# Optimization experiments

Hardware: AMD Instinct MI355X
Metric: run time of the kernel (lower is better)

Reference implementation:

```python
import jax, jax.numpy as jnp
import numpy as np

BETA = 0.5
THR = 1.0
BN_EPS = 1e-5

@jax.custom_vjp
def spike(x):
    # heaviside fire: spk = 1[x > 0]
    return (x > 0).astype(x.dtype)

def _spike_fwd(x):
    return spike(x), x

def _spike_bwd(x, g):
    # snnTorch surrogate.atan(), alpha=2: grad = (alpha/2) / (1 + (pi/2*alpha*x)^2) = 1/(1+(pi*x)^2)
    return (g / (1.0 + (jnp.pi * x) ** 2),)

spike.defvjp(_spike_fwd, _spike_bwd)

def setup_inputs() -> dict:
    key = jax.random.key(0)
    ks = jax.random.split(key, 6)
    B, T, D, O = 512, 128, 512, 10
    data = jax.random.normal(ks[0], (B, T, D), dtype=jnp.float32)
    # deterministic Dropout(0.5) mask in {0, 2} (scaled by 1/keep_prob), time-major
    u = jax.random.uniform(ks[1], (T, B, D), dtype=jnp.float32)
    drop_mask = (u > 0.5).astype(jnp.float32) * 2.0
    W1 = jax.random.normal(ks[2], (D, D), dtype=jnp.float32) / np.sqrt(D)
    b1 = jax.random.normal(ks[3], (D,), dtype=jnp.float32) * 0.01
    gamma = jnp.ones((D,), dtype=jnp.float32)
    bn_beta = jnp.zeros((D,), dtype=jnp.float32)
    W2 = jax.random.normal(ks[4], (O, D), dtype=jnp.float32) / np.sqrt(D)
    b2 = jax.random.normal(ks[5], (O,), dtype=jnp.float32) * 0.01
    return {"data": data, "drop_mask": drop_mask, "W1": W1, "b1": b1,
            "gamma": gamma, "bn_beta": bn_beta, "W2": W2, "b2": b2}

def reference(data, drop_mask, W1, b1, gamma, bn_beta, W2, b2):
    B, T, D = data.shape
    O = W2.shape[0]
    xs = jnp.transpose(data, (1, 0, 2))  # [T, B, D] time-major

    def batchnorm(x):  # training-mode BatchNorm1d over batch dim
        mean = jnp.mean(x, axis=0)
        var = jnp.mean((x - mean) ** 2, axis=0)
        return gamma * (x - mean) * jax.lax.rsqrt(var + BN_EPS) + bn_beta

    def step(carry, inp):
        mem1, spk1, mem2, spk2 = carry
        xt, mt = inp
        cur1 = batchnorm((mt * xt) @ W1.T + b1)          # dropout -> linear -> BN
        mem1 = BETA * mem1 + cur1 - spk1 * THR           # Leaky, subtract reset
        spk1 = spike(mem1 - THR)
        cur2 = spk1 @ W2.T + b2
        mem2 = BETA * mem2 + cur2 - spk2 * THR
        spk2 = spike(mem2 - THR)
        return (mem1, spk1, mem2, spk2), spk2

    init = (jnp.zeros((B, D), data.dtype), jnp.zeros((B, D), data.dtype),
            jnp.zeros((B, O), data.dtype), jnp.zeros((B, O), data.dtype))
    _, spk_rec = jax.lax.scan(step, init, (xs, drop_mask))
    return spk_rec  # [T, B, out_size] == torch.stack(spk_rec)
```

## Files before the change

### kernel.cpp

```cpp
#include <hip/hip_runtime.h>
#include <math.h>

#define B_ 512
#define T_ 128
#define D_ 512
#define O_ 10

typedef unsigned int uint32;
typedef unsigned long long uint64;
typedef short bf16x8 __attribute__((ext_vector_type(8)));
typedef float f32x4 __attribute__((ext_vector_type(4)));

__device__ __forceinline__ uint32 bf16rne(float f) {
    uint32 u = __float_as_uint(f);
    return (u + 0x7FFFu + ((u >> 16) & 1u)) >> 16;
}
__device__ __forceinline__ float bf16f(uint32 h) { return __uint_as_float(h << 16); }

__global__ __launch_bounds__(256)
void presplitW_kernel(const float* __restrict__ W1, unsigned short* __restrict__ Wsp)
{
    const int idx = blockIdx.x * 256 + threadIdx.x;
    const float4 v = *(const float4*)(W1 + (size_t)idx * 4);
    float vv[4] = {v.x, v.y, v.z, v.w};
    uint32 c0[4], c1[4], c2[4];
#pragma unroll
    for (int i = 0; i < 4; ++i) {
        c0[i] = bf16rne(vv[i]);
        float r = vv[i] - bf16f(c0[i]);
        c1[i] = bf16rne(r);
        float r2 = r - bf16f(c1[i]);
        c2[i] = bf16rne(r2);
    }
    const size_t base = (size_t)idx * 4;
    uint2 w;
    w.x = c0[0] | (c0[1] << 16); w.y = c0[2] | (c0[3] << 16);
    *(uint2*)(Wsp + base) = w;
    w.x = c1[0] | (c1[1] << 16); w.y = c1[2] | (c1[3] << 16);
    *(uint2*)(Wsp + 262144 + base) = w;
    w.x = c2[0] | (c2[1] << 16); w.y = c2[2] | (c2[3] << 16);
    *(uint2*)(Wsp + 524288 + base) = w;
}

#define SPW 40
#define SPL (128*SPW)

__global__ __launch_bounds__(256)
void gemm1_kernel(const float* __restrict__ data, const float* __restrict__ drop,
                  const unsigned short* __restrict__ Wsp, const float* __restrict__ b1,
                  float* __restrict__ hbuf, double* __restrict__ pSum,
                  double* __restrict__ pSq, int t0, int Tc)
{
    __shared__ __align__(16) unsigned short As3[3 * SPL];
    __shared__ __align__(16) unsigned short Ws3[3 * SPL];

    const int tid = threadIdx.x;
    const int bid = blockIdx.x;
    const int xcd = bid & 7;
    const int rest = bid >> 3;
    const int yy = rest & 3;
    const int g = (rest >> 2) * 8 + xcd;

    const int R = g * 128;
    const int tc = R >> 9;
    const int b_base = R & 511;
    const int t = t0 + tc;
    const int d0 = yy * 128;

    const int w = tid >> 6;
    const int lane = tid & 63;
    const int wm = w & 1, wn = w >> 1;
    const int q = lane >> 4, r16 = lane & 15;

    f32x4 acc[4][4];
#pragma unroll
    for (int i = 0; i < 4; ++i)
#pragma unroll
        for (int j = 0; j < 4; ++j) acc[i][j] = (f32x4){0.f, 0.f, 0.f, 0.f};

    for (int k0 = 0; k0 < 512; k0 += 32) {
#pragma unroll
        for (int i = 0; i < 2; ++i) {
            const int p = tid + i * 256;
            const int m = p >> 2;
            const int kg = (p & 3) * 8;
            const float* dsrc = data + ((size_t)(b_base + m) * T_ + t) * D_ + k0 + kg;
            const float* msrc = drop + ((size_t)t * B_ + b_base + m) * D_ + k0 + kg;
            const float4 dv0 = *(const float4*)(dsrc);
            const float4 dv1 = *(const float4*)(dsrc + 4);
            const float4 mv0 = *(const float4*)(msrc);
            const float4 mv1 = *(const float4*)(msrc + 4);
            float vv[8] = {dv0.x*mv0.x, dv0.y*mv0.y, dv0.z*mv0.z, dv0.w*mv0.w,
                           dv1.x*mv1.x, dv1.y*mv1.y, dv1.z*mv1.z, dv1.w*mv1.w};
            uint32 u0[8], u1[8], u2[8];
#pragma unroll
            for (int e = 0; e < 8; ++e) {
                u0[e] = bf16rne(vv[e]);
                const float r = vv[e] - bf16f(u0[e]);
                u1[e] = bf16rne(r);
                const float r2 = r - bf16f(u1[e]);
                u2[e] = bf16rne(r2);
            }
            const int dst = m * SPW + kg;
            uint4 pk;
            pk.x = u0[0]|(u0[1]<<16); pk.y = u0[2]|(u0[3]<<16);
            pk.z = u0[4]|(u0[5]<<16); pk.w = u0[6]|(u0[7]<<16);
            *(uint4*)(&As3[dst]) = pk;
            pk.x = u1[0]|(u1[1]<<16); pk.y = u1[2]|(u1[3]<<16);
            pk.z = u1[4]|(u1[5]<<16); pk.w = u1[6]|(u1[7]<<16);
            *(uint4*)(&As3[SPL + dst]) = pk;
            pk.x = u2[0]|(u2[1]<<16); pk.y = u2[2]|(u2[3]<<16);
            pk.z = u2[4]|(u2[5]<<16); pk.w = u2[6]|(u2[7]<<16);
            *(uint4*)(&As3[2*SPL + dst]) = pk;
        }
#pragma unroll
        for (int i = 0; i < 6; ++i) {
            const int p = tid + i * 256;
            const int s = p >> 9;
            const int rem = p & 511;
            const int n = rem >> 2;
            const int kg = (rem & 3) * 8;
            const uint4 pk = *(const uint4*)(Wsp + (size_t)s * 262144
                                             + (size_t)(d0 + n) * 512 + k0 + kg);
            *(uint4*)(&Ws3[s * SPL + n * SPW + kg]) = pk;
        }
        __syncthreads();

        bf16x8 af[4][3], bfr[4][3];
#pragma unroll
        for (int mt = 0; mt < 4; ++mt)
#pragma unroll
            for (int s = 0; s < 3; ++s)
                af[mt][s] = *(const bf16x8*)(&As3[s*SPL + (wm*64 + mt*16 + r16)*SPW + q*8]);
#pragma unroll
        for (int nt = 0; nt < 4; ++nt)
#pragma unroll
            for (int s = 0; s < 3; ++s)
                bfr[nt][s] = *(const bf16x8*)(&Ws3[s*SPL + (wn*64 + nt*16 + r16)*SPW + q*8]);

#define PRODUCT(SA, SB)                                                          \
        {                                                                        \
            _Pragma("unroll")                                                    \
            for (int mt = 0; mt < 4; ++mt) {                                     \
                _Pragma("unroll")                                                \
                for (int nt = 0; nt < 4; ++nt)                                   \
                    acc[mt][nt] = __builtin_amdgcn_mfma_f32_16x16x32_bf16(       \
                        af[mt][SA], bfr[nt][SB], acc[mt][nt], 0, 0, 0);          \
            }                                                                    \
        }
        PRODUCT(0, 0)
        PRODUCT(0, 1)
        PRODUCT(1, 0)
        PRODUCT(1, 1)
        PRODUCT(0, 2)
        PRODUCT(2, 0)
#undef PRODUCT
        __syncthreads();
    }

    float b1c[4];
#pragma unroll
    for (int nt = 0; nt < 4; ++nt) b1c[nt] = b1[d0 + wn*64 + nt*16 + r16];

    double sd[4], sq[4];
#pragma unroll
    for (int nt = 0; nt < 4; ++nt) { sd[nt] = 0.0; sq[nt] = 0.0; }

#pragma unroll
    for (int mt = 0; mt < 4; ++mt)
#pragma unroll
        for (int r = 0; r < 4; ++r) {
            const int row = R + wm*64 + mt*16 + q*4 + r;
            float* op = hbuf + (size_t)row * D_ + d0 + wn*64 + r16;
#pragma unroll
            for (int nt = 0; nt < 4; ++nt) {
                const float hf = acc[mt][nt][r] + b1c[nt];
                op[nt*16] = hf;
                const double dh = (double)hf;
                sd[nt] += dh;
                sq[nt] = fma(dh, dh, sq[nt]);
            }
        }
#pragma unroll
    for (int nt = 0; nt < 4; ++nt) {
        sd[nt] += __shfl_xor(sd[nt], 16); sd[nt] += __shfl_xor(sd[nt], 32);
        sq[nt] += __shfl_xor(sq[nt], 16); sq[nt] += __shfl_xor(sq[nt], 32);
    }
    double* dsh = (double*)&As3[0];
    __syncthreads();
    if (q == 0) {
#pragma unroll
        for (int nt = 0; nt < 4; ++nt) {
            dsh[(w*64 + nt*16 + r16)*2 + 0] = sd[nt];
            dsh[(w*64 + nt*16 + r16)*2 + 1] = sq[nt];
        }
    }
    __syncthreads();
    if (tid < 128) {
        const int col = tid;
        const int gg = col >> 6, c = col & 63;
        const double S = dsh[((2*gg)*64 + c)*2 + 0] + dsh[((2*gg+1)*64 + c)*2 + 0];
        const double Q = dsh[((2*gg)*64 + c)*2 + 1] + dsh[((2*gg+1)*64 + c)*2 + 1];
        const int bt = b_base >> 7;
        pSum[((size_t)(bt*Tc + tc))*D_ + d0 + col] = S;
        pSq [((size_t)(bt*Tc + tc))*D_ + d0 + col] = Q;
    }
}

__global__ __launch_bounds__(256)
void finalize_kernel(const double* __restrict__ pSum, const double* __restrict__ pSq,
                     const float* __restrict__ gamma, const float* __restrict__ bn_beta,
                     float* __restrict__ scaleArr, float* __restrict__ shiftArr, int Tc)
{
    const int tc = blockIdx.x;
    const int d = blockIdx.y * 256 + threadIdx.x;
    double S = 0.0, Q = 0.0;
#pragma unroll
    for (int bt = 0; bt < 4; ++bt) {
        S += pSum[((size_t)(bt * Tc + tc)) * D_ + d];
        Q += pSq [((size_t)(bt * Tc + tc)) * D_ + d];
    }
    const double mean = S / (double)B_;
    const double var  = Q / (double)B_ - mean * mean;
    const double rs   = 1.0 / sqrt(var + 1e-5);
    const double gm   = (double)gamma[d] * rs;
    scaleArr[tc * D_ + d] = (float)gm;
    shiftArr[tc * D_ + d] = (float)((double)bn_beta[d] - gm * mean);
}

__global__ __launch_bounds__(256)
void scanA_kernel(const float* __restrict__ hbuf, const float* __restrict__ scaleArr,
                  const float* __restrict__ shiftArr, uint64* __restrict__ spkM,
                  float* __restrict__ sMem1, float* __restrict__ sSpk1, int t0, int Tc)
{
    const int e = blockIdx.x * 256 + threadIdx.x;
    const int b = e >> 9;
    const int d = e & 511;
    const int lane = threadIdx.x & 63;
    const int mword = (e >> 6);

    float m1, s1;
    if (t0 == 0) { m1 = 0.f; s1 = 0.f; }
    else { m1 = sMem1[e]; s1 = sSpk1[e]; }

    float hv = hbuf[e];
    float sc = scaleArr[d];
    float sf = shiftArr[d];

    for (int tc = 0; tc < Tc; ++tc) {
        float hvN, scN, sfN;
        if (tc + 1 < Tc) {
            hvN = hbuf[(size_t)(tc + 1) * (B_ * D_) + e];
            scN = scaleArr[(tc + 1) * D_ + d];
            sfN = shiftArr[(tc + 1) * D_ + d];
        }
        const float cur1 = fmaf(sc, hv, sf);
        m1 = fmaf(0.5f, m1, cur1) - s1;
        s1 = ((m1 - 1.0f) > 0.f) ? 1.f : 0.f;

        const uint64 mask = __ballot(s1 == 1.f);
        if (lane == 0)
            spkM[(size_t)tc * (B_ * 8) + mword] = mask;

        hv = hvN; sc = scN; sf = sfN;
    }

    sMem1[e] = m1;
    sSpk1[e] = s1;
}

__global__ __launch_bounds__(256)
void gemm2_kernel(const uint64* __restrict__ spkM, const float* __restrict__ W2,
                  const float* __restrict__ b2, float* __restrict__ cur2)
{
    const int tid = threadIdx.x;
    const int w = tid >> 6, lane = tid & 63;
    const int rowBase = blockIdx.x * 16 + w * 4;

    float w2r[O_][8];
#pragma unroll
    for (int o = 0; o < O_; ++o) {
        const float4 wa = *(const float4*)(W2 + o * D_ + lane * 8);
        const float4 wb = *(const float4*)(W2 + o * D_ + lane * 8 + 4);
        w2r[o][0] = wa.x; w2r[o][1] = wa.y; w2r[o][2] = wa.z; w2r[o][3] = wa.w;
        w2r[o][4] = wb.x; w2r[o][5] = wb.y; w2r[o][6] = wb.z; w2r[o][7] = wb.w;
    }
    float b2v[O_];
#pragma unroll
    for (int o = 0; o < O_; ++o) b2v[o] = b2[o];

    for (int rr = 0; rr < 4; ++rr) {
        const int row = rowBase + rr;
        const uint64 mk = spkM[(size_t)row * 8 + (lane >> 3)];
        const uint32 byte = (uint32)(mk >> ((lane & 7) * 8)) & 0xFFu;
        float f[8];
#pragma unroll
        for (int j = 0; j < 8; ++j)
            f[j] = (byte & (1u << j)) ? 1.0f : 0.0f;
        float p[O_];
#pragma unroll
        for (int o = 0; o < O_; ++o) {
            float v = f[0] * w2r[o][0];
#pragma unroll
            for (int j = 1; j < 8; ++j) v = fmaf(f[j], w2r[o][j], v);
            p[o] = v;
        }
#pragma unroll
        for (int o = 0; o < O_; ++o) {
#pragma unroll
            for (int off = 32; off > 0; off >>= 1)
                p[o] += __shfl_xor(p[o], off);
        }
        float outv = 0.f;
#pragma unroll
        for (int o = 0; o < O_; ++o)
            if (lane == o) outv = p[o] + b2v[o];
        if (lane < O_)
            cur2[(size_t)row * O_ + lane] = outv;
    }
}

__global__ __launch_bounds__(256)
void scanB_kernel(const float* __restrict__ cur2, float* __restrict__ out,
                  float* __restrict__ sMem2, float* __restrict__ sSpk2, int t0, int Tc)
{
    const int idx = blockIdx.x * 256 + threadIdx.x;
    float mem2, spk2;
    if (t0 == 0) { mem2 = 0.f; spk2 = 0.f; }
    else { mem2 = sMem2[idx]; spk2 = sSpk2[idx]; }

    float v[4], vn[4];
#pragma unroll
    for (int j = 0; j < 4; ++j) v[j] = cur2[(size_t)j * (B_ * O_) + idx];

    for (int tg = 0; tg < Tc; tg += 4) {
        if (tg + 4 < Tc) {
#pragma unroll
            for (int j = 0; j < 4; ++j)
                vn[j] = cur2[(size_t)(tg + 4 + j) * (B_ * O_) + idx];
        }
#pragma unroll
        for (int j = 0; j < 4; ++j) {
            mem2 = fmaf(0.5f, mem2, v[j]) - spk2;
            spk2 = ((mem2 - 1.0f) > 0.f) ? 1.f : 0.f;
            out[(size_t)(t0 + tg + j) * (B_ * O_) + idx] = spk2;
        }
#pragma unroll
        for (int j = 0; j < 4; ++j) v[j] = vn[j];
    }
    sMem2[idx] = mem2;
    sSpk2[idx] = spk2;
}

extern "C" void kernel_launch(void* const* d_in, const int* in_sizes, int n_in,
                              void* d_out, int out_size, void* d_ws, size_t ws_size,
                              hipStream_t stream) {
    const float* data    = (const float*)d_in[0];
    const float* drop    = (const float*)d_in[1];
    const float* W1      = (const float*)d_in[2];
    const float* b1      = (const float*)d_in[3];
    const float* gamma   = (const float*)d_in[4];
    const float* bn_beta = (const float*)d_in[5];
    const float* W2      = (const float*)d_in[6];
    const float* b2      = (const float*)d_in[7];
    float* out = (float*)d_out;

    const size_t fixedBytes = 1572864 + 2*1048576 + 2*20480;
    const size_t perT = 1048576 + 32768 + 20480 + 4096 + 32768;
    int Tc = T_;
    while (Tc > 2 && fixedBytes + (size_t)Tc * perT > ws_size) Tc >>= 1;

    char* p = (char*)d_ws;
    double* pSum    = (double*)p; p += (size_t)4 * Tc * D_ * 8;
    double* pSq     = (double*)p; p += (size_t)4 * Tc * D_ * 8;
    float* hbuf     = (float*)p; p += (size_t)Tc * B_ * D_ * 4;
    float* scaleArr = (float*)p; p += (size_t)Tc * D_ * 4;
    float* shiftArr = (float*)p; p += (size_t)Tc * D_ * 4;
    float* sMem1    = (float*)p; p += (size_t)B_ * D_ * 4;
    float* sSpk1    = (float*)p; p += (size_t)B_ * D_ * 4;
    float* sMem2    = (float*)p; p += (size_t)B_ * O_ * 4;
    float* sSpk2    = (float*)p; p += (size_t)B_ * O_ * 4;
    float* cur2     = (float*)p; p += (size_t)Tc * B_ * O_ * 4;
    unsigned short* Wsp = (unsigned short*)p; p += (size_t)3 * D_ * D_ * 2;
    uint64* spkM    = (uint64*)p; p += (size_t)Tc * B_ * 8 * 8;

    presplitW_kernel<<<256, 256, 0, stream>>>(W1, Wsp);

    for (int t0 = 0; t0 < T_; t0 += Tc) {
        gemm1_kernel<<<Tc * 16, 256, 0, stream>>>(data, drop, Wsp, b1, hbuf,
                                                  pSum, pSq, t0, Tc);
        finalize_kernel<<<dim3(Tc, D_ / 256), 256, 0, stream>>>(
            pSum, pSq, gamma, bn_beta, scaleArr, shiftArr, Tc);
        scanA_kernel<<<(B_ * D_) / 256, 256, 0, stream>>>(hbuf, scaleArr, shiftArr, spkM,
                                                          sMem1, sSpk1, t0, Tc);
        gemm2_kernel<<<Tc * 32, 256, 0, stream>>>(spkM, W2, b2, cur2);
        scanB_kernel<<<20, 256, 0, stream>>>(cur2, out, sMem2, sSpk2, t0, Tc);
    }
}
```

Measured before the change: 541.5 us.

## Swizzle gemm1 LDS tiles, batch scanA prefetch, and restructure gemm2 reduction

The gemm1 LDS row pitch drops from 40 to 32 halfwords and an XOR swizzle on the 8-element group index replaces the padding, which saves shared memory while avoiding bank conflicts. scanA now prefetches four timesteps of hbuf/scale/shift at a time instead of one, to get more loads in flight. gemm2 is reorganised so each thread handles one eighth of a row across eight column chunks, reading W2 directly and reducing with three shuffles instead of six. Its grid is halved accordingly. The trade-offs are extra W2 global/L1 traffic per thread and higher register pressure from the P[8][10] array.

```diff
diff --git a/kernel.cpp b/kernel.cpp
--- a/kernel.cpp
+++ b/kernel.cpp
@@ -42,7 +42,7 @@
     *(uint2*)(Wsp + 524288 + base) = w;
 }
 
-#define SPW 40
+#define SPW 32
 #define SPL (128*SPW)
 
 __global__ __launch_bounds__(256)
@@ -83,7 +83,8 @@
         for (int i = 0; i < 2; ++i) {
             const int p = tid + i * 256;
             const int m = p >> 2;
-            const int kg = (p & 3) * 8;
+            const int qg = p & 3;
+            const int kg = qg * 8;
             const float* dsrc = data + ((size_t)(b_base + m) * T_ + t) * D_ + k0 + kg;
             const float* msrc = drop + ((size_t)t * B_ + b_base + m) * D_ + k0 + kg;
             const float4 dv0 = *(const float4*)(dsrc);
@@ -101,7 +102,8 @@
                 const float r2 = r - bf16f(u1[e]);
                 u2[e] = bf16rne(r2);
             }
-            const int dst = m * SPW + kg;
+            const int qs = qg ^ ((m >> 1) & 3);
+            const int dst = m * SPW + qs * 8;
             uint4 pk;
             pk.x = u0[0]|(u0[1]<<16); pk.y = u0[2]|(u0[3]<<16);
             pk.z = u0[4]|(u0[5]<<16); pk.w = u0[6]|(u0[7]<<16);
@@ -119,24 +121,27 @@
             const int s = p >> 9;
             const int rem = p & 511;
             const int n = rem >> 2;
-            const int kg = (rem & 3) * 8;
+            const int qg = rem & 3;
+            const int kg = qg * 8;
             const uint4 pk = *(const uint4*)(Wsp + (size_t)s * 262144
                                              + (size_t)(d0 + n) * 512 + k0 + kg);
-            *(uint4*)(&Ws3[s * SPL + n * SPW + kg]) = pk;
+            const int qs = qg ^ ((n >> 1) & 3);
+            *(uint4*)(&Ws3[s * SPL + n * SPW + qs * 8]) = pk;
         }
         __syncthreads();
 
+        const int qa = q ^ ((r16 >> 1) & 3);
         bf16x8 af[4][3], bfr[4][3];
 #pragma unroll
         for (int mt = 0; mt < 4; ++mt)
 #pragma unroll
             for (int s = 0; s < 3; ++s)
-                af[mt][s] = *(const bf16x8*)(&As3[s*SPL + (wm*64 + mt*16 + r16)*SPW + q*8]);
+                af[mt][s] = *(const bf16x8*)(&As3[s*SPL + (wm*64 + mt*16 + r16)*SPW + qa*8]);
 #pragma unroll
         for (int nt = 0; nt < 4; ++nt)
 #pragma unroll
             for (int s = 0; s < 3; ++s)
-                bfr[nt][s] = *(const bf16x8*)(&Ws3[s*SPL + (wn*64 + nt*16 + r16)*SPW + q*8]);
+                bfr[nt][s] = *(const bf16x8*)(&Ws3[s*SPL + (wn*64 + nt*16 + r16)*SPW + qa*8]);
 
 #define PRODUCT(SA, SB)                                                          \
         {                                                                        \
@@ -234,7 +239,6 @@
                   float* __restrict__ sMem1, float* __restrict__ sSpk1, int t0, int Tc)
 {
     const int e = blockIdx.x * 256 + threadIdx.x;
-    const int b = e >> 9;
     const int d = e & 511;
     const int lane = threadIdx.x & 63;
     const int mword = (e >> 6);
@@ -243,26 +247,37 @@
     if (t0 == 0) { m1 = 0.f; s1 = 0.f; }
     else { m1 = sMem1[e]; s1 = sSpk1[e]; }
 
-    float hv = hbuf[e];
-    float sc = scaleArr[d];
-    float sf = shiftArr[d];
-
-    for (int tc = 0; tc < Tc; ++tc) {
-        float hvN, scN, sfN;
-        if (tc + 1 < Tc) {
-            hvN = hbuf[(size_t)(tc + 1) * (B_ * D_) + e];
-            scN = scaleArr[(tc + 1) * D_ + d];
-            sfN = shiftArr[(tc + 1) * D_ + d];
-        }
-        const float cur1 = fmaf(sc, hv, sf);
-        m1 = fmaf(0.5f, m1, cur1) - s1;
-        s1 = ((m1 - 1.0f) > 0.f) ? 1.f : 0.f;
-
-        const uint64 mask = __ballot(s1 == 1.f);
-        if (lane == 0)
-            spkM[(size_t)tc * (B_ * 8) + mword] = mask;
-
-        hv = hvN; sc = scN; sf = sfN;
+    float hv[4], sc[4], sf[4];
+#pragma unroll
+    for (int j = 0; j < 4; ++j) {
+        const int tcj = (j < Tc) ? j : (Tc - 1);
+        hv[j] = hbuf[(size_t)tcj * (B_ * D_) + e];
+        sc[j] = scaleArr[tcj * D_ + d];
+        sf[j] = shiftArr[tcj * D_ + d];
+    }
+
+    for (int tc = 0; tc < Tc; tc += 4) {
+        float hvN[4], scN[4], sfN[4];
+#pragma unroll
+        for (int j = 0; j < 4; ++j) {
+            int tn = tc + 4 + j; tn = (tn < Tc) ? tn : (Tc - 1);
+            hvN[j] = hbuf[(size_t)tn * (B_ * D_) + e];
+            scN[j] = scaleArr[tn * D_ + d];
+            sfN[j] = shiftArr[tn * D_ + d];
+        }
+#pragma unroll
+        for (int j = 0; j < 4; ++j) {
+            if (tc + j < Tc) {
+                const float cur1 = fmaf(sc[j], hv[j], sf[j]);
+                m1 = fmaf(0.5f, m1, cur1) - s1;
+                s1 = ((m1 - 1.0f) > 0.f) ? 1.f : 0.f;
+                const uint64 mask = __ballot(s1 == 1.f);
+                if (lane == 0)
+                    spkM[(size_t)(tc + j) * (B_ * 8) + mword] = mask;
+            }
+        }
+#pragma unroll
+        for (int j = 0; j < 4; ++j) { hv[j] = hvN[j]; sc[j] = scN[j]; sf[j] = sfN[j]; }
     }
 
     sMem1[e] = m1;
@@ -273,51 +288,57 @@
 void gemm2_kernel(const uint64* __restrict__ spkM, const float* __restrict__ W2,
                   const float* __restrict__ b2, float* __restrict__ cur2)
 {
-    const int tid = threadIdx.x;
-    const int w = tid >> 6, lane = tid & 63;
-    const int rowBase = blockIdx.x * 16 + w * 4;
-
-    float w2r[O_][8];
-#pragma unroll
-    for (int o = 0; o < O_; ++o) {
-        const float4 wa = *(const float4*)(W2 + o * D_ + lane * 8);
-        const float4 wb = *(const float4*)(W2 + o * D_ + lane * 8 + 4);
-        w2r[o][0] = wa.x; w2r[o][1] = wa.y; w2r[o][2] = wa.z; w2r[o][3] = wa.w;
-        w2r[o][4] = wb.x; w2r[o][5] = wb.y; w2r[o][6] = wb.z; w2r[o][7] = wb.w;
-    }
-    float b2v[O_];
-#pragma unroll
-    for (int o = 0; o < O_; ++o) b2v[o] = b2[o];
-
-    for (int rr = 0; rr < 4; ++rr) {
-        const int row = rowBase + rr;
-        const uint64 mk = spkM[(size_t)row * 8 + (lane >> 3)];
-        const uint32 byte = (uint32)(mk >> ((lane & 7) * 8)) & 0xFFu;
+    const int g = blockIdx.x * 256 + threadIdx.x;
+    const int row = g >> 3;
+    const int i = g & 7;
+    const unsigned char* sp = (const unsigned char*)spkM;
+
+    float P[8][O_];
+#pragma unroll
+    for (int c = 0; c < 8; ++c) {
+        const uint32 byte = sp[(size_t)row * 64 + c * 8 + i];
         float f[8];
 #pragma unroll
         for (int j = 0; j < 8; ++j)
             f[j] = (byte & (1u << j)) ? 1.0f : 0.0f;
-        float p[O_];
 #pragma unroll
         for (int o = 0; o < O_; ++o) {
-            float v = f[0] * w2r[o][0];
-#pragma unroll
-            for (int j = 1; j < 8; ++j) v = fmaf(f[j], w2r[o][j], v);
-            p[o] = v;
-        }
-#pragma unroll
-        for (int o = 0; o < O_; ++o) {
-#pragma unroll
-            for (int off = 32; off > 0; off >>= 1)
-                p[o] += __shfl_xor(p[o], off);
-        }
-        float outv = 0.f;
-#pragma unroll
-        for (int o = 0; o < O_; ++o)
-            if (lane == o) outv = p[o] + b2v[o];
-        if (lane < O_)
-            cur2[(size_t)row * O_ + lane] = outv;
-    }
+            const float* wp = W2 + o * D_ + (i + 8 * c) * 8;
+            const float4 wa = *(const float4*)(wp);
+            const float4 wb = *(const float4*)(wp + 4);
+            float v = f[0] * wa.x;
+            v = fmaf(f[1], wa.y, v); v = fmaf(f[2], wa.z, v); v = fmaf(f[3], wa.w, v);
+            v = fmaf(f[4], wb.x, v); v = fmaf(f[5], wb.y, v); v = fmaf(f[6], wb.z, v);
+            v = fmaf(f[7], wb.w, v);
+            P[c][o] = v;
+        }
+    }
+
+    float p[O_];
+#pragma unroll
+    for (int o = 0; o < O_; ++o) {
+        const float a1 = P[0][o] + P[4][o];
+        const float a2 = P[2][o] + P[6][o];
+        const float a3 = P[1][o] + P[5][o];
+        const float a4 = P[3][o] + P[7][o];
+        p[o] = (a1 + a2) + (a3 + a4);
+    }
+#pragma unroll
+    for (int o = 0; o < O_; ++o) {
+        p[o] += __shfl_xor(p[o], 4);
+        p[o] += __shfl_xor(p[o], 2);
+        p[o] += __shfl_xor(p[o], 1);
+    }
+
+    float out0 = 0.f, out1 = 0.f;
+#pragma unroll
+    for (int o = 0; o < 8; ++o)
+        if (i == o) out0 = p[o] + b2[o];
+    if (i == 0) out1 = p[8] + b2[8];
+    if (i == 1) out1 = p[9] + b2[9];
+    cur2[(size_t)row * O_ + i] = out0;
+    if (i < 2)
+        cur2[(size_t)row * O_ + 8 + i] = out1;
 }
 
 __global__ __launch_bounds__(256)
@@ -393,7 +414,7 @@
             pSum, pSq, gamma, bn_beta, scaleArr, shiftArr, Tc);
         scanA_kernel<<<(B_ * D_) / 256, 256, 0, stream>>>(hbuf, scaleArr, shiftArr, spkM,
                                                           sMem1, sSpk1, t0, Tc);
-        gemm2_kernel<<<Tc * 32, 256, 0, stream>>>(spkM, W2, b2, cur2);
+        gemm2_kernel<<<Tc * 16, 256, 0, stream>>>(spkM, W2, b2, cur2);
         scanB_kernel<<<20, 256, 0, stream>>>(cur2, out, sMem2, sSpk2, t0, Tc);
     }
 }
```

New measurement: 510.9 us. 1.06x faster.
